# Kernel tuning notes

Measured on AMD Instinct MI355X. Metric: run time of the kernel, lower is better.

Reference implementation:

```python
import jax, jax.numpy as jnp
import numpy as np

N_HEADS = 16


def setup_inputs() -> dict:
    key = jax.random.key(0)
    k1, k2, k3, k4 = jax.random.split(key, 4)
    b, s, d = 2, 2048, 1024
    x = jax.random.normal(k1, (b, s, d), dtype=jnp.float32)
    attn_B = jax.random.normal(k2, (b, N_HEADS, s, s), dtype=jnp.float32) * 0.02
    W_attn = jax.random.normal(k3, (d, 3 * d), dtype=jnp.float32) * (1.0 / np.sqrt(d))
    b_attn = jax.random.normal(k4, (3 * d,), dtype=jnp.float32) * 0.01
    return {"x": x, "attn_B": attn_B, "W_attn": W_attn, "b_attn": b_attn}


def reference(x, attn_B, W_attn, b_attn):
    b, s, d = x.shape
    h = N_HEADS
    hd = d // h
    qkv = x @ W_attn + b_attn                       # [b, s, 3d]
    Q, K, V = jnp.split(qkv, 3, axis=-1)
    # [b, s, d] -> [b, h, s, hd]
    Q = Q.reshape(b, s, h, hd).transpose(0, 2, 1, 3)
    K = K.reshape(b, s, h, hd).transpose(0, 2, 1, 3)
    V = V.reshape(b, s, h, hd).transpose(0, 2, 1, 3)
    scale = 1.0 / jnp.sqrt(jnp.asarray(hd, dtype=Q.dtype))
    scores = jnp.einsum("bhqk,bhsk->bhqs", Q, K) * scale   # [b, h, s, s]
    attn = jax.nn.softmax(scores, axis=-1) + attn_B          # post-softmax additive bias
    y = jnp.einsum("bhqs,bhsd->bhqd", attn, V)               # [b, h, s, hd]
    y = y.transpose(0, 2, 1, 3).reshape(b, s, d)
    return y
```

## Files before the change

kernel.cpp:

```cpp
#include <hip/hip_runtime.h>
#include <hip/hip_bf16.h>


typedef __attribute__((ext_vector_type(4))) float  f32x4;
typedef __attribute__((ext_vector_type(8))) short  bf16x8;
typedef __attribute__((ext_vector_type(4))) short  s16x4;
typedef __attribute__((ext_vector_type(4))) unsigned u32x4;

__device__ __forceinline__ short f2bf(float f) {
    __hip_bfloat16 h = __float2bfloat16(f);
    return __builtin_bit_cast(short, h);
}

__device__ __forceinline__ unsigned cvt_pk_bf16(float lo, float hi) {
    unsigned w;
    asm("v_cvt_pk_bf16_f32 %0, %1, %2" : "=v"(w) : "v"(lo), "v"(hi));
    return w;
}

__device__ __forceinline__ void gll16(const short* g, short* l) {
    __builtin_amdgcn_global_load_lds(
        (const __attribute__((address_space(1))) void*)g,
        (__attribute__((address_space(3))) void*)l, 16, 0, 0);
}

__global__ void conv_x_kernel(const float* __restrict__ x, short* __restrict__ xb) {
    int idx = blockIdx.x * 256 + threadIdx.x;
    f32x4 v = *reinterpret_cast<const f32x4*>(x + (size_t)idx * 4);
    s16x4 o;
    o[0] = f2bf(v[0]); o[1] = f2bf(v[1]); o[2] = f2bf(v[2]); o[3] = f2bf(v[3]);
    *reinterpret_cast<s16x4*>(xb + (size_t)idx * 4) = o;
}

__global__ void wtrans_kernel(const float* __restrict__ W, short* __restrict__ Wt) {
    __shared__ float tile[64][65];
    int kb = blockIdx.x, nb = blockIdx.y;
    int t = threadIdx.x;
    int c4 = (t & 15) * 4;
    int r0 = t >> 4;
#pragma unroll
    for (int rr = 0; rr < 4; ++rr) {
        int kl = r0 + rr * 16;
        f32x4 v = *reinterpret_cast<const f32x4*>(W + (size_t)(kb * 64 + kl) * 3072 + nb * 64 + c4);
        tile[kl][c4 + 0] = v[0]; tile[kl][c4 + 1] = v[1];
        tile[kl][c4 + 2] = v[2]; tile[kl][c4 + 3] = v[3];
    }
    __syncthreads();
#pragma unroll
    for (int rr = 0; rr < 4; ++rr) {
        int nl = r0 + rr * 16;
        s16x4 o;
#pragma unroll
        for (int i = 0; i < 4; ++i) o[i] = f2bf(tile[c4 + i][nl]);
        *reinterpret_cast<s16x4*>(Wt + (size_t)(nb * 64 + nl) * 1024 + kb * 64 + c4) = o;
    }
}

__global__ __launch_bounds__(256) void qkv_gemm_kernel(
    const short* __restrict__ xb, const short* __restrict__ Wt,
    const float* __restrict__ bias,
    short* __restrict__ Qo, short* __restrict__ Ko, short* __restrict__ Vo)
{
    __shared__ short As[128 * 64];
    __shared__ short Bs[128 * 64];
    int tid = threadIdx.x;
    int wave = tid >> 6, lane = tid & 63, g = lane >> 4, lr = lane & 15;
    int wr = wave >> 1, wc = wave & 1;
    int bm = blockIdx.x, bn = blockIdx.y;

    f32x4 acc[4][4];
#pragma unroll
    for (int a = 0; a < 4; ++a)
#pragma unroll
        for (int b = 0; b < 4; ++b) acc[a][b] = (f32x4){0.f, 0.f, 0.f, 0.f};

    for (int k0 = 0; k0 < 1024; k0 += 64) {
#pragma unroll
        for (int j = 0; j < 4; ++j) {
            int c = j * 256 + tid;
            int row = c >> 3, cc = c & 7;
            int scc = (cc ^ (row & 7)) * 8;
            gll16(xb + (size_t)(bm * 128 + row) * 1024 + k0 + scc,
                  &As[(j * 256 + wave * 64) * 8]);
            gll16(Wt + (size_t)(bn * 128 + row) * 1024 + k0 + scc,
                  &Bs[(j * 256 + wave * 64) * 8]);
        }
        __syncthreads();

        bf16x8 af[2][4], bfr[2][4];
#pragma unroll
        for (int mt = 0; mt < 4; ++mt) {
            int row = wr * 64 + mt * 16 + lr;
            af[0][mt] = *reinterpret_cast<const bf16x8*>(&As[row * 64 + (((g    ) ^ (lr & 7)) * 8)]);
            af[1][mt] = *reinterpret_cast<const bf16x8*>(&As[row * 64 + (((g + 4) ^ (lr & 7)) * 8)]);
        }
#pragma unroll
        for (int nt = 0; nt < 4; ++nt) {
            int row = wc * 64 + nt * 16 + lr;
            bfr[0][nt] = *reinterpret_cast<const bf16x8*>(&Bs[row * 64 + (((g    ) ^ (lr & 7)) * 8)]);
            bfr[1][nt] = *reinterpret_cast<const bf16x8*>(&Bs[row * 64 + (((g + 4) ^ (lr & 7)) * 8)]);
        }
#pragma unroll
        for (int mt = 0; mt < 4; ++mt)
#pragma unroll
            for (int nt = 0; nt < 4; ++nt) {
                acc[mt][nt] = __builtin_amdgcn_mfma_f32_16x16x32_bf16(af[0][mt], bfr[0][nt], acc[mt][nt], 0, 0, 0);
                acc[mt][nt] = __builtin_amdgcn_mfma_f32_16x16x32_bf16(af[1][mt], bfr[1][nt], acc[mt][nt], 0, 0, 0);
            }
        __syncthreads();
    }

#pragma unroll
    for (int nt = 0; nt < 4; ++nt) {
        int n = bn * 128 + wc * 64 + nt * 16 + lr;
        float bv = bias[n];
        int which = n >> 10;
        int h = (n >> 6) & 15;
        int dd = n & 63;
        short* base = (which == 0) ? Qo : (which == 1) ? Ko : Vo;
#pragma unroll
        for (int mt = 0; mt < 4; ++mt) {
#pragma unroll
            for (int r = 0; r < 4; ++r) {
                int m = bm * 128 + wr * 64 + mt * 16 + g * 4 + r;
                int bb = m >> 11, s = m & 2047;
                float v = acc[mt][nt][r] + bv;
                base[(((size_t)bb * 16 + h) * 2048 + s) * 64 + dd] = f2bf(v);
            }
        }
    }
}

__global__ __launch_bounds__(256) void vtrans_kernel(const short* __restrict__ V, short* __restrict__ Vt) {
    __shared__ short t[64][72];
    int st = blockIdx.x, bh = blockIdx.y;
    int tid = threadIdx.x;
#pragma unroll
    for (int j = 0; j < 2; ++j) {
        int c = j * 256 + tid;
        int row = c >> 3, cc = c & 7;
        bf16x8 v = *reinterpret_cast<const bf16x8*>(V + (size_t)((bh * 2048) + st * 64 + row) * 64 + cc * 8);
        *reinterpret_cast<bf16x8*>(&t[row][cc * 8]) = v;
    }
    __syncthreads();
#pragma unroll
    for (int j = 0; j < 2; ++j) {
        int c = j * 256 + tid;
        int d = c >> 3, cs = c & 7;
        bf16x8 o;
#pragma unroll
        for (int i = 0; i < 8; ++i) o[i] = t[cs * 8 + i][d];
        *reinterpret_cast<bf16x8*>(Vt + (size_t)(bh * 64 + d) * 2048 + st * 64 + cs * 8) = o;
    }
}

__global__ __launch_bounds__(512, 4) void attn_kernel(
    const short* __restrict__ Qw, const short* __restrict__ Kw, const short* __restrict__ Vtw,
    const float* __restrict__ attnB, float* __restrict__ out)
{
    __shared__ short Ks [2][64 * 64];
    __shared__ short Vts[2][64 * 64];
    __shared__ short Ps [8][16 * 64];

    int id = blockIdx.x;
    int bh3 = id & 7;
    int qt  = (id >> 3) & 15;
    int bh  = ((id >> 7) << 3) | bh3;
    int b = bh >> 4, h = bh & 15;
    int tid = threadIdx.x;
    int wave = tid >> 6, lane = tid & 63, g = lane >> 4, lr = lane & 15;

    const short* Qb = Qw  + (size_t)bh * 2048 * 64;
    const short* Kb = Kw  + (size_t)bh * 2048 * 64;
    const short* Vb = Vtw + (size_t)bh * 64 * 2048;
    const float* Bp = attnB + (size_t)bh * 2048 * 2048;

    int qbase = qt * 128 + wave * 16;

    bf16x8 qf0, qf1;
    {
        const short* qp = Qb + (size_t)(qbase + lr) * 64 + g * 8;
        qf0 = *reinterpret_cast<const bf16x8*>(qp);
        qf1 = *reinterpret_cast<const bf16x8*>(qp + 32);
    }
    const float* brow = Bp + (size_t)(qbase + lr) * 2048 + g * 8;

    f32x4 Os[4], Ob[4];
#pragma unroll
    for (int dt = 0; dt < 4; ++dt) { Os[dt] = (f32x4){0.f,0.f,0.f,0.f}; Ob[dt] = (f32x4){0.f,0.f,0.f,0.f}; }
    float lsum = 0.f;

#define STAGE_KV(buf, ktt) do {                                                   \
    int row = tid >> 3, cc = tid & 7;                                             \
    int scc = (cc ^ (row & 7)) * 8;                                               \
    gll16(Kb + (size_t)((ktt) * 64 + row) * 64 + scc,                             \
          &Ks[buf][wave * 512]);                                                  \
    gll16(Vb + (size_t)row * 2048 + (ktt) * 64 + scc,                             \
          &Vts[buf][wave * 512]);                                                 \
} while (0)

    f32x4 bfn0, bfn1, bfn2, bfn3;
    STAGE_KV(0, 0);
    __builtin_amdgcn_sched_barrier(0);
    bfn0 = __builtin_nontemporal_load(reinterpret_cast<const f32x4*>(brow));
    bfn1 = __builtin_nontemporal_load(reinterpret_cast<const f32x4*>(brow + 4));
    bfn2 = __builtin_nontemporal_load(reinterpret_cast<const f32x4*>(brow + 32));
    bfn3 = __builtin_nontemporal_load(reinterpret_cast<const f32x4*>(brow + 36));
    asm volatile("s_waitcnt vmcnt(4)" ::: "memory");
    __builtin_amdgcn_s_barrier();
    __builtin_amdgcn_sched_barrier(0);

    for (int kt = 0; kt < 32; ++kt) {
        int cur = kt & 1;

        unsigned bb0 = cvt_pk_bf16(bfn0[0], bfn0[1]);
        unsigned bb1 = cvt_pk_bf16(bfn0[2], bfn0[3]);
        unsigned bb2 = cvt_pk_bf16(bfn1[0], bfn1[1]);
        unsigned bb3 = cvt_pk_bf16(bfn1[2], bfn1[3]);
        unsigned bb4 = cvt_pk_bf16(bfn2[0], bfn2[1]);
        unsigned bb5 = cvt_pk_bf16(bfn2[2], bfn2[3]);
        unsigned bb6 = cvt_pk_bf16(bfn3[0], bfn3[1]);
        unsigned bb7 = cvt_pk_bf16(bfn3[2], bfn3[3]);

        if (kt < 31) {
            STAGE_KV(cur ^ 1, kt + 1);
            __builtin_amdgcn_sched_barrier(0);
            const float* bp = brow + (kt + 1) * 64;
            bfn0 = __builtin_nontemporal_load(reinterpret_cast<const f32x4*>(bp));
            bfn1 = __builtin_nontemporal_load(reinterpret_cast<const f32x4*>(bp + 4));
            bfn2 = __builtin_nontemporal_load(reinterpret_cast<const f32x4*>(bp + 32));
            bfn3 = __builtin_nontemporal_load(reinterpret_cast<const f32x4*>(bp + 36));
        }

        f32x4 S[4];
        __builtin_amdgcn_s_setprio(1);
#pragma unroll
        for (int nt = 0; nt < 4; ++nt) {
            int row = nt * 16 + lr;
            bf16x8 kf0 = *reinterpret_cast<const bf16x8*>(&Ks[cur][row * 64 + (((g    ) ^ (lr & 7)) * 8)]);
            bf16x8 kf1 = *reinterpret_cast<const bf16x8*>(&Ks[cur][row * 64 + (((g + 4) ^ (lr & 7)) * 8)]);
            f32x4 s = (f32x4){0.f,0.f,0.f,0.f};
            s = __builtin_amdgcn_mfma_f32_16x16x32_bf16(kf0, qf0, s, 0, 0, 0);
            s = __builtin_amdgcn_mfma_f32_16x16x32_bf16(kf1, qf1, s, 0, 0, 0);
            S[nt] = s;
        }
        __builtin_amdgcn_s_setprio(0);

#pragma unroll
        for (int nt = 0; nt < 4; ++nt)
#pragma unroll
            for (int r = 0; r < 4; ++r) {
                float p = exp2f(S[nt][r] * 0.1803368801111f);
                S[nt][r] = p;
                lsum += p;
            }

        short* psw = &Ps[wave][lr * 64];
#pragma unroll
        for (int nt = 0; nt < 4; ++nt)
#pragma unroll
            for (int rp = 0; rp < 2; ++rp) {
                unsigned w = cvt_pk_bf16(S[nt][2 * rp], S[nt][2 * rp + 1]);
                int kp = 8 * nt + 2 * g + rp;
                int bi = kp >> 2, off = kp & 3;
                *reinterpret_cast<unsigned*>(psw + ((bi ^ (lr & 7)) << 3) + off * 2) = w;
            }

        bf16x8 pf0 = *reinterpret_cast<const bf16x8*>(&Ps[wave][lr * 64 + (((g    ) ^ (lr & 7)) * 8)]);
        bf16x8 pf1 = *reinterpret_cast<const bf16x8*>(&Ps[wave][lr * 64 + (((g + 4) ^ (lr & 7)) * 8)]);
        bf16x8 bbf0, bbf1;
        {
            u32x4 t0 = (u32x4){bb0, bb1, bb2, bb3};
            u32x4 t1 = (u32x4){bb4, bb5, bb6, bb7};
            bbf0 = __builtin_bit_cast(bf16x8, t0);
            bbf1 = __builtin_bit_cast(bf16x8, t1);
        }

        __builtin_amdgcn_s_setprio(1);
#pragma unroll
        for (int dt = 0; dt < 4; ++dt) {
            int row = dt * 16 + lr;
            bf16x8 v0 = *reinterpret_cast<const bf16x8*>(&Vts[cur][row * 64 + (((g    ) ^ (lr & 7)) * 8)]);
            bf16x8 v1 = *reinterpret_cast<const bf16x8*>(&Vts[cur][row * 64 + (((g + 4) ^ (lr & 7)) * 8)]);
            Os[dt] = __builtin_amdgcn_mfma_f32_16x16x32_bf16(pf0,  v0, Os[dt], 0, 0, 0);
            Os[dt] = __builtin_amdgcn_mfma_f32_16x16x32_bf16(pf1,  v1, Os[dt], 0, 0, 0);
            Ob[dt] = __builtin_amdgcn_mfma_f32_16x16x32_bf16(bbf0, v0, Ob[dt], 0, 0, 0);
            Ob[dt] = __builtin_amdgcn_mfma_f32_16x16x32_bf16(bbf1, v1, Ob[dt], 0, 0, 0);
        }
        __builtin_amdgcn_s_setprio(0);

        if (kt < 31) {
            asm volatile("s_waitcnt vmcnt(4)" ::: "memory");
            __builtin_amdgcn_s_barrier();
            __builtin_amdgcn_sched_barrier(0);
        }
    }
#undef STAGE_KV

    float l = lsum;
    l += __shfl_xor(l, 16);
    l += __shfl_xor(l, 32);
    float inv = 1.0f / l;
#pragma unroll
    for (int r = 0; r < 4; ++r) {
        float invr = __shfl(inv, g * 4 + r);
        int q = qbase + g * 4 + r;
#pragma unroll
        for (int dt = 0; dt < 4; ++dt) {
            int dcol = dt * 16 + lr;
            float v = Os[dt][r] * invr + Ob[dt][r];
            __builtin_nontemporal_store(v, &out[((size_t)(b * 2048 + q) * 16 + h) * 64 + dcol]);
        }
    }
}

extern "C" void kernel_launch(void* const* d_in, const int* in_sizes, int n_in,
                              void* d_out, int out_size, void* d_ws, size_t ws_size,
                              hipStream_t stream) {
    const float* x     = (const float*)d_in[0];
    const float* attnB = (const float*)d_in[1];
    const float* W     = (const float*)d_in[2];
    const float* bias  = (const float*)d_in[3];
    float* out = (float*)d_out;

    short* ws = (short*)d_ws;
    short* xb = ws;
    short* Wt = xb + 4194304;
    short* Q  = Wt + 3145728;
    short* K  = Q  + 4194304;
    short* V  = K  + 4194304;
    short* Vt = V  + 4194304;

    conv_x_kernel<<<4096, 256, 0, stream>>>(x, xb);
    wtrans_kernel<<<dim3(16, 48), 256, 0, stream>>>(W, Wt);
    qkv_gemm_kernel<<<dim3(32, 24), 256, 0, stream>>>(xb, Wt, bias, Q, K, V);
    vtrans_kernel<<<dim3(32, 32), 256, 0, stream>>>(V, Vt);
    attn_kernel<<<512, 512, 0, stream>>>(Q, K, Vt, attnB, out);
}
```

Measured before the change: 205.5 us.

## Split bias-times-V product into separate blocks of a heterogeneous fused launch

The attention kernel previously streamed the large fp32 attn_B tensor inside the softmax loop and did the B·V MFMAs alongside P·V. Now one launch of 768 blocks runs two kinds of work. The first 512 blocks do only the softmax attention, and the other 256 blocks do the bias·V product as a plain GEMM into a workspace buffer. A new add kernel then sums the two outputs. This aims to decouple the bandwidth-bound bias stream from the compute-bound attention so they overlap across CUs, at the cost of an extra output round trip and one more launch.

```diff
diff --git a/kernel.cpp b/kernel.cpp
--- a/kernel.cpp
+++ b/kernel.cpp
@@ -16,6 +16,12 @@
     unsigned w;
     asm("v_cvt_pk_bf16_f32 %0, %1, %2" : "=v"(w) : "v"(lo), "v"(hi));
     return w;
+}
+
+__device__ __forceinline__ bf16x8 pack8(f32x4 a, f32x4 b) {
+    u32x4 t = (u32x4){cvt_pk_bf16(a[0], a[1]), cvt_pk_bf16(a[2], a[3]),
+                      cvt_pk_bf16(b[0], b[1]), cvt_pk_bf16(b[2], b[3])};
+    return __builtin_bit_cast(bf16x8, t);
 }
 
 __device__ __forceinline__ void gll16(const short* g, short* l) {
@@ -154,164 +160,234 @@
     }
 }
 
-__global__ __launch_bounds__(512, 4) void attn_kernel(
+__global__ __launch_bounds__(512, 4) void fused_kernel(
     const short* __restrict__ Qw, const short* __restrict__ Kw, const short* __restrict__ Vtw,
-    const float* __restrict__ attnB, float* __restrict__ out)
+    const float* __restrict__ attnB, float* __restrict__ out, float* __restrict__ Obuf)
 {
     __shared__ short Ks [2][64 * 64];
     __shared__ short Vts[2][64 * 64];
     __shared__ short Ps [8][16 * 64];
 
     int id = blockIdx.x;
-    int bh3 = id & 7;
-    int qt  = (id >> 3) & 15;
-    int bh  = ((id >> 7) << 3) | bh3;
-    int b = bh >> 4, h = bh & 15;
     int tid = threadIdx.x;
     int wave = tid >> 6, lane = tid & 63, g = lane >> 4, lr = lane & 15;
 
-    const short* Qb = Qw  + (size_t)bh * 2048 * 64;
-    const short* Kb = Kw  + (size_t)bh * 2048 * 64;
-    const short* Vb = Vtw + (size_t)bh * 64 * 2048;
-    const float* Bp = attnB + (size_t)bh * 2048 * 2048;
-
-    int qbase = qt * 128 + wave * 16;
-
-    bf16x8 qf0, qf1;
-    {
-        const short* qp = Qb + (size_t)(qbase + lr) * 64 + g * 8;
-        qf0 = *reinterpret_cast<const bf16x8*>(qp);
-        qf1 = *reinterpret_cast<const bf16x8*>(qp + 32);
-    }
-    const float* brow = Bp + (size_t)(qbase + lr) * 2048 + g * 8;
-
-    f32x4 Os[4], Ob[4];
-#pragma unroll
-    for (int dt = 0; dt < 4; ++dt) { Os[dt] = (f32x4){0.f,0.f,0.f,0.f}; Ob[dt] = (f32x4){0.f,0.f,0.f,0.f}; }
-    float lsum = 0.f;
+    if (id < 512) {
+        int bh3 = id & 7;
+        int qt  = (id >> 3) & 15;
+        int bh  = ((id >> 7) << 3) | bh3;
+        int b = bh >> 4, h = bh & 15;
+
+        const short* Qb = Qw  + (size_t)bh * 2048 * 64;
+        const short* Kb = Kw  + (size_t)bh * 2048 * 64;
+        const short* Vb = Vtw + (size_t)bh * 64 * 2048;
+
+        int qbase = qt * 128 + wave * 16;
+
+        bf16x8 qf0, qf1;
+        {
+            const short* qp = Qb + (size_t)(qbase + lr) * 64 + g * 8;
+            qf0 = *reinterpret_cast<const bf16x8*>(qp);
+            qf1 = *reinterpret_cast<const bf16x8*>(qp + 32);
+        }
+
+        f32x4 Os[4];
+#pragma unroll
+        for (int dt = 0; dt < 4; ++dt) Os[dt] = (f32x4){0.f,0.f,0.f,0.f};
+        float lsum = 0.f;
 
 #define STAGE_KV(buf, ktt) do {                                                   \
-    int row = tid >> 3, cc = tid & 7;                                             \
-    int scc = (cc ^ (row & 7)) * 8;                                               \
-    gll16(Kb + (size_t)((ktt) * 64 + row) * 64 + scc,                             \
-          &Ks[buf][wave * 512]);                                                  \
-    gll16(Vb + (size_t)row * 2048 + (ktt) * 64 + scc,                             \
-          &Vts[buf][wave * 512]);                                                 \
-} while (0)
-
-    f32x4 bfn0, bfn1, bfn2, bfn3;
-    STAGE_KV(0, 0);
-    __builtin_amdgcn_sched_barrier(0);
-    bfn0 = __builtin_nontemporal_load(reinterpret_cast<const f32x4*>(brow));
-    bfn1 = __builtin_nontemporal_load(reinterpret_cast<const f32x4*>(brow + 4));
-    bfn2 = __builtin_nontemporal_load(reinterpret_cast<const f32x4*>(brow + 32));
-    bfn3 = __builtin_nontemporal_load(reinterpret_cast<const f32x4*>(brow + 36));
-    asm volatile("s_waitcnt vmcnt(4)" ::: "memory");
-    __builtin_amdgcn_s_barrier();
-    __builtin_amdgcn_sched_barrier(0);
-
-    for (int kt = 0; kt < 32; ++kt) {
-        int cur = kt & 1;
-
-        unsigned bb0 = cvt_pk_bf16(bfn0[0], bfn0[1]);
-        unsigned bb1 = cvt_pk_bf16(bfn0[2], bfn0[3]);
-        unsigned bb2 = cvt_pk_bf16(bfn1[0], bfn1[1]);
-        unsigned bb3 = cvt_pk_bf16(bfn1[2], bfn1[3]);
-        unsigned bb4 = cvt_pk_bf16(bfn2[0], bfn2[1]);
-        unsigned bb5 = cvt_pk_bf16(bfn2[2], bfn2[3]);
-        unsigned bb6 = cvt_pk_bf16(bfn3[0], bfn3[1]);
-        unsigned bb7 = cvt_pk_bf16(bfn3[2], bfn3[3]);
-
-        if (kt < 31) {
-            STAGE_KV(cur ^ 1, kt + 1);
+        int row = tid >> 3, cc = tid & 7;                                         \
+        int scc = (cc ^ (row & 7)) * 8;                                           \
+        gll16(Kb + (size_t)((ktt) * 64 + row) * 64 + scc,                         \
+              &Ks[buf][wave * 512]);                                              \
+        gll16(Vb + (size_t)row * 2048 + (ktt) * 64 + scc,                         \
+              &Vts[buf][wave * 512]);                                             \
+    } while (0)
+
+        STAGE_KV(0, 0);
+        asm volatile("s_waitcnt vmcnt(0)" ::: "memory");
+        __builtin_amdgcn_s_barrier();
+        __builtin_amdgcn_sched_barrier(0);
+
+        for (int kt = 0; kt < 32; ++kt) {
+            int cur = kt & 1;
+            if (kt < 31) STAGE_KV(cur ^ 1, kt + 1);
             __builtin_amdgcn_sched_barrier(0);
-            const float* bp = brow + (kt + 1) * 64;
-            bfn0 = __builtin_nontemporal_load(reinterpret_cast<const f32x4*>(bp));
-            bfn1 = __builtin_nontemporal_load(reinterpret_cast<const f32x4*>(bp + 4));
-            bfn2 = __builtin_nontemporal_load(reinterpret_cast<const f32x4*>(bp + 32));
-            bfn3 = __builtin_nontemporal_load(reinterpret_cast<const f32x4*>(bp + 36));
-        }
-
-        f32x4 S[4];
-        __builtin_amdgcn_s_setprio(1);
-#pragma unroll
-        for (int nt = 0; nt < 4; ++nt) {
-            int row = nt * 16 + lr;
-            bf16x8 kf0 = *reinterpret_cast<const bf16x8*>(&Ks[cur][row * 64 + (((g    ) ^ (lr & 7)) * 8)]);
-            bf16x8 kf1 = *reinterpret_cast<const bf16x8*>(&Ks[cur][row * 64 + (((g + 4) ^ (lr & 7)) * 8)]);
-            f32x4 s = (f32x4){0.f,0.f,0.f,0.f};
-            s = __builtin_amdgcn_mfma_f32_16x16x32_bf16(kf0, qf0, s, 0, 0, 0);
-            s = __builtin_amdgcn_mfma_f32_16x16x32_bf16(kf1, qf1, s, 0, 0, 0);
-            S[nt] = s;
-        }
-        __builtin_amdgcn_s_setprio(0);
-
-#pragma unroll
-        for (int nt = 0; nt < 4; ++nt)
-#pragma unroll
-            for (int r = 0; r < 4; ++r) {
-                float p = exp2f(S[nt][r] * 0.1803368801111f);
-                S[nt][r] = p;
-                lsum += p;
-            }
-
-        short* psw = &Ps[wave][lr * 64];
-#pragma unroll
-        for (int nt = 0; nt < 4; ++nt)
-#pragma unroll
-            for (int rp = 0; rp < 2; ++rp) {
-                unsigned w = cvt_pk_bf16(S[nt][2 * rp], S[nt][2 * rp + 1]);
-                int kp = 8 * nt + 2 * g + rp;
-                int bi = kp >> 2, off = kp & 3;
-                *reinterpret_cast<unsigned*>(psw + ((bi ^ (lr & 7)) << 3) + off * 2) = w;
-            }
-
-        bf16x8 pf0 = *reinterpret_cast<const bf16x8*>(&Ps[wave][lr * 64 + (((g    ) ^ (lr & 7)) * 8)]);
-        bf16x8 pf1 = *reinterpret_cast<const bf16x8*>(&Ps[wave][lr * 64 + (((g + 4) ^ (lr & 7)) * 8)]);
-        bf16x8 bbf0, bbf1;
-        {
-            u32x4 t0 = (u32x4){bb0, bb1, bb2, bb3};
-            u32x4 t1 = (u32x4){bb4, bb5, bb6, bb7};
-            bbf0 = __builtin_bit_cast(bf16x8, t0);
-            bbf1 = __builtin_bit_cast(bf16x8, t1);
-        }
-
-        __builtin_amdgcn_s_setprio(1);
-#pragma unroll
-        for (int dt = 0; dt < 4; ++dt) {
-            int row = dt * 16 + lr;
-            bf16x8 v0 = *reinterpret_cast<const bf16x8*>(&Vts[cur][row * 64 + (((g    ) ^ (lr & 7)) * 8)]);
-            bf16x8 v1 = *reinterpret_cast<const bf16x8*>(&Vts[cur][row * 64 + (((g + 4) ^ (lr & 7)) * 8)]);
-            Os[dt] = __builtin_amdgcn_mfma_f32_16x16x32_bf16(pf0,  v0, Os[dt], 0, 0, 0);
-            Os[dt] = __builtin_amdgcn_mfma_f32_16x16x32_bf16(pf1,  v1, Os[dt], 0, 0, 0);
-            Ob[dt] = __builtin_amdgcn_mfma_f32_16x16x32_bf16(bbf0, v0, Ob[dt], 0, 0, 0);
-            Ob[dt] = __builtin_amdgcn_mfma_f32_16x16x32_bf16(bbf1, v1, Ob[dt], 0, 0, 0);
-        }
-        __builtin_amdgcn_s_setprio(0);
-
-        if (kt < 31) {
-            asm volatile("s_waitcnt vmcnt(4)" ::: "memory");
-            __builtin_amdgcn_s_barrier();
-            __builtin_amdgcn_sched_barrier(0);
-        }
-    }
+
+            f32x4 S[4];
+            __builtin_amdgcn_s_setprio(1);
+#pragma unroll
+            for (int nt = 0; nt < 4; ++nt) {
+                int row = nt * 16 + lr;
+                bf16x8 kf0 = *reinterpret_cast<const bf16x8*>(&Ks[cur][row * 64 + (((g    ) ^ (lr & 7)) * 8)]);
+                bf16x8 kf1 = *reinterpret_cast<const bf16x8*>(&Ks[cur][row * 64 + (((g + 4) ^ (lr & 7)) * 8)]);
+                f32x4 s = (f32x4){0.f,0.f,0.f,0.f};
+                s = __builtin_amdgcn_mfma_f32_16x16x32_bf16(kf0, qf0, s, 0, 0, 0);
+                s = __builtin_amdgcn_mfma_f32_16x16x32_bf16(kf1, qf1, s, 0, 0, 0);
+                S[nt] = s;
+            }
+            __builtin_amdgcn_s_setprio(0);
+
+#pragma unroll
+            for (int nt = 0; nt < 4; ++nt)
+#pragma unroll
+                for (int r = 0; r < 4; ++r) {
+                    float p = exp2f(S[nt][r] * 0.1803368801111f);
+                    S[nt][r] = p;
+                    lsum += p;
+                }
+
+            short* psw = &Ps[wave][lr * 64];
+#pragma unroll
+            for (int nt = 0; nt < 4; ++nt)
+#pragma unroll
+                for (int rp = 0; rp < 2; ++rp) {
+                    unsigned w = cvt_pk_bf16(S[nt][2 * rp], S[nt][2 * rp + 1]);
+                    int kp = 8 * nt + 2 * g + rp;
+                    int bi = kp >> 2, off = kp & 3;
+                    *reinterpret_cast<unsigned*>(psw + ((bi ^ (lr & 7)) << 3) + off * 2) = w;
+                }
+
+            bf16x8 pf0 = *reinterpret_cast<const bf16x8*>(&Ps[wave][lr * 64 + (((g    ) ^ (lr & 7)) * 8)]);
+            bf16x8 pf1 = *reinterpret_cast<const bf16x8*>(&Ps[wave][lr * 64 + (((g + 4) ^ (lr & 7)) * 8)]);
+
+            __builtin_amdgcn_s_setprio(1);
+#pragma unroll
+            for (int dt = 0; dt < 4; ++dt) {
+                int row = dt * 16 + lr;
+                bf16x8 v0 = *reinterpret_cast<const bf16x8*>(&Vts[cur][row * 64 + (((g    ) ^ (lr & 7)) * 8)]);
+                bf16x8 v1 = *reinterpret_cast<const bf16x8*>(&Vts[cur][row * 64 + (((g + 4) ^ (lr & 7)) * 8)]);
+                Os[dt] = __builtin_amdgcn_mfma_f32_16x16x32_bf16(pf0, v0, Os[dt], 0, 0, 0);
+                Os[dt] = __builtin_amdgcn_mfma_f32_16x16x32_bf16(pf1, v1, Os[dt], 0, 0, 0);
+            }
+            __builtin_amdgcn_s_setprio(0);
+
+            if (kt < 31) {
+                asm volatile("s_waitcnt vmcnt(0)" ::: "memory");
+                __builtin_amdgcn_s_barrier();
+                __builtin_amdgcn_sched_barrier(0);
+            }
+        }
 #undef STAGE_KV
 
-    float l = lsum;
-    l += __shfl_xor(l, 16);
-    l += __shfl_xor(l, 32);
-    float inv = 1.0f / l;
-#pragma unroll
-    for (int r = 0; r < 4; ++r) {
-        float invr = __shfl(inv, g * 4 + r);
-        int q = qbase + g * 4 + r;
-#pragma unroll
-        for (int dt = 0; dt < 4; ++dt) {
-            int dcol = dt * 16 + lr;
-            float v = Os[dt][r] * invr + Ob[dt][r];
-            __builtin_nontemporal_store(v, &out[((size_t)(b * 2048 + q) * 16 + h) * 64 + dcol]);
-        }
-    }
+        float l = lsum;
+        l += __shfl_xor(l, 16);
+        l += __shfl_xor(l, 32);
+        float inv = 1.0f / l;
+#pragma unroll
+        for (int r = 0; r < 4; ++r) {
+            float invr = __shfl(inv, g * 4 + r);
+            int q = qbase + g * 4 + r;
+#pragma unroll
+            for (int dt = 0; dt < 4; ++dt) {
+                int dcol = dt * 16 + lr;
+                out[((size_t)(b * 2048 + q) * 16 + h) * 64 + dcol] = Os[dt][r] * invr;
+            }
+        }
+    } else {
+        int j = id - 512;
+        int bh = ((j >> 6) << 3) | (j & 7);
+        int qt2 = (j >> 3) & 7;
+        int b = bh >> 4, h = bh & 15;
+        int qb = qt2 * 256;
+
+        const float* Bp = attnB + (size_t)bh * 2048 * 2048;
+        const short* Vb = Vtw + (size_t)bh * 64 * 2048;
+        const float* br0 = Bp + (size_t)(qb + wave * 32 + lr) * 2048 + g * 8;
+        const float* br1 = br0 + (size_t)16 * 2048;
+
+        f32x4 acc[2][4];
+#pragma unroll
+        for (int mt = 0; mt < 2; ++mt)
+#pragma unroll
+            for (int nt = 0; nt < 4; ++nt) acc[mt][nt] = (f32x4){0.f,0.f,0.f,0.f};
+
+#define STAGE_V(buf, ktt) do {                                                    \
+        int row = tid >> 3, cc = tid & 7;                                         \
+        int scc = (cc ^ (row & 7)) * 8;                                           \
+        gll16(Vb + (size_t)row * 2048 + (ktt) * 64 + scc,                         \
+              &Ks[buf][wave * 512]);                                              \
+    } while (0)
+
+        f32x4 b00, b01, b02, b03, b10, b11, b12, b13;
+        STAGE_V(0, 0);
+        __builtin_amdgcn_sched_barrier(0);
+        b00 = __builtin_nontemporal_load(reinterpret_cast<const f32x4*>(br0));
+        b01 = __builtin_nontemporal_load(reinterpret_cast<const f32x4*>(br0 + 4));
+        b02 = __builtin_nontemporal_load(reinterpret_cast<const f32x4*>(br0 + 32));
+        b03 = __builtin_nontemporal_load(reinterpret_cast<const f32x4*>(br0 + 36));
+        b10 = __builtin_nontemporal_load(reinterpret_cast<const f32x4*>(br1));
+        b11 = __builtin_nontemporal_load(reinterpret_cast<const f32x4*>(br1 + 4));
+        b12 = __builtin_nontemporal_load(reinterpret_cast<const f32x4*>(br1 + 32));
+        b13 = __builtin_nontemporal_load(reinterpret_cast<const f32x4*>(br1 + 36));
+        asm volatile("s_waitcnt vmcnt(8)" ::: "memory");
+        __builtin_amdgcn_s_barrier();
+        __builtin_amdgcn_sched_barrier(0);
+
+        for (int kt = 0; kt < 32; ++kt) {
+            int cur = kt & 1;
+
+            bf16x8 a00 = pack8(b00, b01);
+            bf16x8 a01 = pack8(b02, b03);
+            bf16x8 a10 = pack8(b10, b11);
+            bf16x8 a11 = pack8(b12, b13);
+
+            if (kt < 31) {
+                STAGE_V(cur ^ 1, kt + 1);
+                __builtin_amdgcn_sched_barrier(0);
+                const float* p0 = br0 + (kt + 1) * 64;
+                const float* p1 = br1 + (kt + 1) * 64;
+                b00 = __builtin_nontemporal_load(reinterpret_cast<const f32x4*>(p0));
+                b01 = __builtin_nontemporal_load(reinterpret_cast<const f32x4*>(p0 + 4));
+                b02 = __builtin_nontemporal_load(reinterpret_cast<const f32x4*>(p0 + 32));
+                b03 = __builtin_nontemporal_load(reinterpret_cast<const f32x4*>(p0 + 36));
+                b10 = __builtin_nontemporal_load(reinterpret_cast<const f32x4*>(p1));
+                b11 = __builtin_nontemporal_load(reinterpret_cast<const f32x4*>(p1 + 4));
+                b12 = __builtin_nontemporal_load(reinterpret_cast<const f32x4*>(p1 + 32));
+                b13 = __builtin_nontemporal_load(reinterpret_cast<const f32x4*>(p1 + 36));
+            }
+
+            __builtin_amdgcn_s_setprio(1);
+#pragma unroll
+            for (int nt = 0; nt < 4; ++nt) {
+                int row = nt * 16 + lr;
+                bf16x8 v0 = *reinterpret_cast<const bf16x8*>(&Ks[cur][row * 64 + (((g    ) ^ (lr & 7)) * 8)]);
+                bf16x8 v1 = *reinterpret_cast<const bf16x8*>(&Ks[cur][row * 64 + (((g + 4) ^ (lr & 7)) * 8)]);
+                acc[0][nt] = __builtin_amdgcn_mfma_f32_16x16x32_bf16(a00, v0, acc[0][nt], 0, 0, 0);
+                acc[0][nt] = __builtin_amdgcn_mfma_f32_16x16x32_bf16(a01, v1, acc[0][nt], 0, 0, 0);
+                acc[1][nt] = __builtin_amdgcn_mfma_f32_16x16x32_bf16(a10, v0, acc[1][nt], 0, 0, 0);
+                acc[1][nt] = __builtin_amdgcn_mfma_f32_16x16x32_bf16(a11, v1, acc[1][nt], 0, 0, 0);
+            }
+            __builtin_amdgcn_s_setprio(0);
+
+            if (kt < 31) {
+                asm volatile("s_waitcnt vmcnt(8)" ::: "memory");
+                __builtin_amdgcn_s_barrier();
+                __builtin_amdgcn_sched_barrier(0);
+            }
+        }
+#undef STAGE_V
+
+#pragma unroll
+        for (int mt = 0; mt < 2; ++mt)
+#pragma unroll
+            for (int nt = 0; nt < 4; ++nt)
+#pragma unroll
+                for (int r = 0; r < 4; ++r) {
+                    int q = qb + wave * 32 + mt * 16 + g * 4 + r;
+                    int d = nt * 16 + lr;
+                    Obuf[((size_t)(b * 2048 + q) * 16 + h) * 64 + d] = acc[mt][nt][r];
+                }
+    }
+}
+
+__global__ void add_kernel(float* __restrict__ out, const float* __restrict__ Obuf) {
+    int idx = blockIdx.x * 256 + threadIdx.x;
+    f32x4 a = *reinterpret_cast<const f32x4*>(out + (size_t)idx * 4);
+    f32x4 c = *reinterpret_cast<const f32x4*>(Obuf + (size_t)idx * 4);
+    a[0] += c[0]; a[1] += c[1]; a[2] += c[2]; a[3] += c[3];
+    *reinterpret_cast<f32x4*>(out + (size_t)idx * 4) = a;
 }
 
 extern "C" void kernel_launch(void* const* d_in, const int* in_sizes, int n_in,
@@ -330,10 +406,12 @@
     short* K  = Q  + 4194304;
     short* V  = K  + 4194304;
     short* Vt = V  + 4194304;
+    float* Obuf = (float*)(Vt + 4194304);
 
     conv_x_kernel<<<4096, 256, 0, stream>>>(x, xb);
     wtrans_kernel<<<dim3(16, 48), 256, 0, stream>>>(W, Wt);
     qkv_gemm_kernel<<<dim3(32, 24), 256, 0, stream>>>(xb, Wt, bias, Q, K, V);
     vtrans_kernel<<<dim3(32, 32), 256, 0, stream>>>(V, Vt);
-    attn_kernel<<<512, 512, 0, stream>>>(Q, K, Vt, attnB, out);
-}
+    fused_kernel<<<768, 512, 0, stream>>>(Q, K, Vt, attnB, out, Obuf);
+    add_kernel<<<4096, 256, 0, stream>>>(out, Obuf);
+}
```

New measurement: 264.5 us. 28.7% more time.

## Fuse V transpose into QKV GEMM epilogue and deepen bias prefetch in attention

Applied to the files above, without the earlier changes.

The QKV GEMM epilogue now writes V directly in transposed [bh, d, s] layout using 4-element vector stores, so the separate vtrans kernel launch and its extra round trip through memory go away. The attention loop is unrolled by two with static buffer indices, and the attn_B bias tiles are prefetched two iterations ahead using regular loads instead of nontemporal ones. This is meant to hide the bias memory latency better. The cost is more live registers under launch_bounds(512,4), and the vmcnt accounting becomes more delicate.

```diff
diff --git a/kernel.cpp b/kernel.cpp
--- a/kernel.cpp
+++ b/kernel.cpp
@@ -16,6 +16,12 @@
     unsigned w;
     asm("v_cvt_pk_bf16_f32 %0, %1, %2" : "=v"(w) : "v"(lo), "v"(hi));
     return w;
+}
+
+__device__ __forceinline__ bf16x8 pack8(f32x4 a, f32x4 b) {
+    u32x4 t = (u32x4){cvt_pk_bf16(a[0], a[1]), cvt_pk_bf16(a[2], a[3]),
+                      cvt_pk_bf16(b[0], b[1]), cvt_pk_bf16(b[2], b[3])};
+    return __builtin_bit_cast(bf16x8, t);
 }
 
 __device__ __forceinline__ void gll16(const short* g, short* l) {
@@ -59,7 +65,7 @@
 __global__ __launch_bounds__(256) void qkv_gemm_kernel(
     const short* __restrict__ xb, const short* __restrict__ Wt,
     const float* __restrict__ bias,
-    short* __restrict__ Qo, short* __restrict__ Ko, short* __restrict__ Vo)
+    short* __restrict__ Qo, short* __restrict__ Ko, short* __restrict__ Vto)
 {
     __shared__ short As[128 * 64];
     __shared__ short Bs[128 * 64];
@@ -117,40 +123,24 @@
         int which = n >> 10;
         int h = (n >> 6) & 15;
         int dd = n & 63;
-        short* base = (which == 0) ? Qo : (which == 1) ? Ko : Vo;
 #pragma unroll
         for (int mt = 0; mt < 4; ++mt) {
-#pragma unroll
-            for (int r = 0; r < 4; ++r) {
-                int m = bm * 128 + wr * 64 + mt * 16 + g * 4 + r;
-                int bb = m >> 11, s = m & 2047;
-                float v = acc[mt][nt][r] + bv;
-                base[(((size_t)bb * 16 + h) * 2048 + s) * 64 + dd] = f2bf(v);
-            }
-        }
-    }
-}
-
-__global__ __launch_bounds__(256) void vtrans_kernel(const short* __restrict__ V, short* __restrict__ Vt) {
-    __shared__ short t[64][72];
-    int st = blockIdx.x, bh = blockIdx.y;
-    int tid = threadIdx.x;
-#pragma unroll
-    for (int j = 0; j < 2; ++j) {
-        int c = j * 256 + tid;
-        int row = c >> 3, cc = c & 7;
-        bf16x8 v = *reinterpret_cast<const bf16x8*>(V + (size_t)((bh * 2048) + st * 64 + row) * 64 + cc * 8);
-        *reinterpret_cast<bf16x8*>(&t[row][cc * 8]) = v;
-    }
-    __syncthreads();
-#pragma unroll
-    for (int j = 0; j < 2; ++j) {
-        int c = j * 256 + tid;
-        int d = c >> 3, cs = c & 7;
-        bf16x8 o;
-#pragma unroll
-        for (int i = 0; i < 8; ++i) o[i] = t[cs * 8 + i][d];
-        *reinterpret_cast<bf16x8*>(Vt + (size_t)(bh * 64 + d) * 2048 + st * 64 + cs * 8) = o;
+            int m0 = bm * 128 + wr * 64 + mt * 16 + g * 4;
+            int bb = m0 >> 11, s0 = m0 & 2047;
+            if (which == 2) {
+                s16x4 o;
+#pragma unroll
+                for (int r = 0; r < 4; ++r) o[r] = f2bf(acc[mt][nt][r] + bv);
+                *reinterpret_cast<s16x4*>(
+                    Vto + ((size_t)(bb * 16 + h) * 64 + dd) * 2048 + s0) = o;
+            } else {
+                short* base = (which == 0) ? Qo : Ko;
+#pragma unroll
+                for (int r = 0; r < 4; ++r)
+                    base[(((size_t)bb * 16 + h) * 2048 + s0 + r) * 64 + dd] =
+                        f2bf(acc[mt][nt][r] + bv);
+            }
+        }
     }
 }
 
@@ -199,103 +189,110 @@
           &Vts[buf][wave * 512]);                                                 \
 } while (0)
 
-    f32x4 bfn0, bfn1, bfn2, bfn3;
+#define LOADB(d0, d1, d2, d3, ktt) do {                                           \
+    const float* bp_ = brow + (size_t)(ktt) * 64;                                 \
+    d0 = *reinterpret_cast<const f32x4*>(bp_);                                    \
+    d1 = *reinterpret_cast<const f32x4*>(bp_ + 4);                                \
+    d2 = *reinterpret_cast<const f32x4*>(bp_ + 32);                               \
+    d3 = *reinterpret_cast<const f32x4*>(bp_ + 36);                               \
+} while (0)
+
+#define COMPUTE(cur, xb0, xb1) do {                                               \
+    f32x4 S[4];                                                                   \
+    __builtin_amdgcn_s_setprio(1);                                                \
+    _Pragma("unroll")                                                             \
+    for (int nt = 0; nt < 4; ++nt) {                                              \
+        int row = nt * 16 + lr;                                                   \
+        bf16x8 kf0 = *reinterpret_cast<const bf16x8*>(&Ks[cur][row * 64 + (((g    ) ^ (lr & 7)) * 8)]); \
+        bf16x8 kf1 = *reinterpret_cast<const bf16x8*>(&Ks[cur][row * 64 + (((g + 4) ^ (lr & 7)) * 8)]); \
+        f32x4 s = (f32x4){0.f,0.f,0.f,0.f};                                       \
+        s = __builtin_amdgcn_mfma_f32_16x16x32_bf16(kf0, qf0, s, 0, 0, 0);        \
+        s = __builtin_amdgcn_mfma_f32_16x16x32_bf16(kf1, qf1, s, 0, 0, 0);        \
+        S[nt] = s;                                                                \
+    }                                                                             \
+    __builtin_amdgcn_s_setprio(0);                                                \
+    _Pragma("unroll")                                                             \
+    for (int nt = 0; nt < 4; ++nt)                                                \
+        _Pragma("unroll")                                                         \
+        for (int r = 0; r < 4; ++r) {                                             \
+            float p = exp2f(S[nt][r] * 0.1803368801111f);                         \
+            S[nt][r] = p;                                                         \
+            lsum += p;                                                            \
+        }                                                                         \
+    short* psw = &Ps[wave][lr * 64];                                              \
+    _Pragma("unroll")                                                             \
+    for (int nt = 0; nt < 4; ++nt)                                                \
+        _Pragma("unroll")                                                         \
+        for (int rp = 0; rp < 2; ++rp) {                                          \
+            unsigned w = cvt_pk_bf16(S[nt][2 * rp], S[nt][2 * rp + 1]);           \
+            int kp = 8 * nt + 2 * g + rp;                                         \
+            int bi = kp >> 2, off = kp & 3;                                       \
+            *reinterpret_cast<unsigned*>(psw + ((bi ^ (lr & 7)) << 3) + off * 2) = w; \
+        }                                                                         \
+    bf16x8 pf0 = *reinterpret_cast<const bf16x8*>(&Ps[wave][lr * 64 + (((g    ) ^ (lr & 7)) * 8)]); \
+    bf16x8 pf1 = *reinterpret_cast<const bf16x8*>(&Ps[wave][lr * 64 + (((g + 4) ^ (lr & 7)) * 8)]); \
+    __builtin_amdgcn_s_setprio(1);                                                \
+    _Pragma("unroll")                                                             \
+    for (int dt = 0; dt < 4; ++dt) {                                              \
+        int row = dt * 16 + lr;                                                   \
+        bf16x8 v0 = *reinterpret_cast<const bf16x8*>(&Vts[cur][row * 64 + (((g    ) ^ (lr & 7)) * 8)]); \
+        bf16x8 v1 = *reinterpret_cast<const bf16x8*>(&Vts[cur][row * 64 + (((g + 4) ^ (lr & 7)) * 8)]); \
+        Os[dt] = __builtin_amdgcn_mfma_f32_16x16x32_bf16(pf0, v0, Os[dt], 0, 0, 0); \
+        Os[dt] = __builtin_amdgcn_mfma_f32_16x16x32_bf16(pf1, v1, Os[dt], 0, 0, 0); \
+        Ob[dt] = __builtin_amdgcn_mfma_f32_16x16x32_bf16(xb0, v0, Ob[dt], 0, 0, 0); \
+        Ob[dt] = __builtin_amdgcn_mfma_f32_16x16x32_bf16(xb1, v1, Ob[dt], 0, 0, 0); \
+    }                                                                             \
+    __builtin_amdgcn_s_setprio(0);                                                \
+} while (0)
+
+    f32x4 a0, a1, a2, a3, p0, p1, p2, p3;
+
     STAGE_KV(0, 0);
     __builtin_amdgcn_sched_barrier(0);
-    bfn0 = __builtin_nontemporal_load(reinterpret_cast<const f32x4*>(brow));
-    bfn1 = __builtin_nontemporal_load(reinterpret_cast<const f32x4*>(brow + 4));
-    bfn2 = __builtin_nontemporal_load(reinterpret_cast<const f32x4*>(brow + 32));
-    bfn3 = __builtin_nontemporal_load(reinterpret_cast<const f32x4*>(brow + 36));
-    asm volatile("s_waitcnt vmcnt(4)" ::: "memory");
+    LOADB(a0, a1, a2, a3, 0);
+    LOADB(p0, p1, p2, p3, 1);
+    __builtin_amdgcn_sched_barrier(0);
+    asm volatile("s_waitcnt vmcnt(8)" ::: "memory");
     __builtin_amdgcn_s_barrier();
     __builtin_amdgcn_sched_barrier(0);
 
-    for (int kt = 0; kt < 32; ++kt) {
-        int cur = kt & 1;
-
-        unsigned bb0 = cvt_pk_bf16(bfn0[0], bfn0[1]);
-        unsigned bb1 = cvt_pk_bf16(bfn0[2], bfn0[3]);
-        unsigned bb2 = cvt_pk_bf16(bfn1[0], bfn1[1]);
-        unsigned bb3 = cvt_pk_bf16(bfn1[2], bfn1[3]);
-        unsigned bb4 = cvt_pk_bf16(bfn2[0], bfn2[1]);
-        unsigned bb5 = cvt_pk_bf16(bfn2[2], bfn2[3]);
-        unsigned bb6 = cvt_pk_bf16(bfn3[0], bfn3[1]);
-        unsigned bb7 = cvt_pk_bf16(bfn3[2], bfn3[3]);
-
-        if (kt < 31) {
-            STAGE_KV(cur ^ 1, kt + 1);
+    for (int t = 0; t < 16; ++t) {
+        {
+            bf16x8 bbf0 = pack8(a0, a1);
+            bf16x8 bbf1 = pack8(a2, a3);
+            STAGE_KV(1, 2 * t + 1);
             __builtin_amdgcn_sched_barrier(0);
-            const float* bp = brow + (kt + 1) * 64;
-            bfn0 = __builtin_nontemporal_load(reinterpret_cast<const f32x4*>(bp));
-            bfn1 = __builtin_nontemporal_load(reinterpret_cast<const f32x4*>(bp + 4));
-            bfn2 = __builtin_nontemporal_load(reinterpret_cast<const f32x4*>(bp + 32));
-            bfn3 = __builtin_nontemporal_load(reinterpret_cast<const f32x4*>(bp + 36));
-        }
-
-        f32x4 S[4];
-        __builtin_amdgcn_s_setprio(1);
-#pragma unroll
-        for (int nt = 0; nt < 4; ++nt) {
-            int row = nt * 16 + lr;
-            bf16x8 kf0 = *reinterpret_cast<const bf16x8*>(&Ks[cur][row * 64 + (((g    ) ^ (lr & 7)) * 8)]);
-            bf16x8 kf1 = *reinterpret_cast<const bf16x8*>(&Ks[cur][row * 64 + (((g + 4) ^ (lr & 7)) * 8)]);
-            f32x4 s = (f32x4){0.f,0.f,0.f,0.f};
-            s = __builtin_amdgcn_mfma_f32_16x16x32_bf16(kf0, qf0, s, 0, 0, 0);
-            s = __builtin_amdgcn_mfma_f32_16x16x32_bf16(kf1, qf1, s, 0, 0, 0);
-            S[nt] = s;
-        }
-        __builtin_amdgcn_s_setprio(0);
-
-#pragma unroll
-        for (int nt = 0; nt < 4; ++nt)
-#pragma unroll
-            for (int r = 0; r < 4; ++r) {
-                float p = exp2f(S[nt][r] * 0.1803368801111f);
-                S[nt][r] = p;
-                lsum += p;
-            }
-
-        short* psw = &Ps[wave][lr * 64];
-#pragma unroll
-        for (int nt = 0; nt < 4; ++nt)
-#pragma unroll
-            for (int rp = 0; rp < 2; ++rp) {
-                unsigned w = cvt_pk_bf16(S[nt][2 * rp], S[nt][2 * rp + 1]);
-                int kp = 8 * nt + 2 * g + rp;
-                int bi = kp >> 2, off = kp & 3;
-                *reinterpret_cast<unsigned*>(psw + ((bi ^ (lr & 7)) << 3) + off * 2) = w;
-            }
-
-        bf16x8 pf0 = *reinterpret_cast<const bf16x8*>(&Ps[wave][lr * 64 + (((g    ) ^ (lr & 7)) * 8)]);
-        bf16x8 pf1 = *reinterpret_cast<const bf16x8*>(&Ps[wave][lr * 64 + (((g + 4) ^ (lr & 7)) * 8)]);
-        bf16x8 bbf0, bbf1;
-        {
-            u32x4 t0 = (u32x4){bb0, bb1, bb2, bb3};
-            u32x4 t1 = (u32x4){bb4, bb5, bb6, bb7};
-            bbf0 = __builtin_bit_cast(bf16x8, t0);
-            bbf1 = __builtin_bit_cast(bf16x8, t1);
-        }
-
-        __builtin_amdgcn_s_setprio(1);
-#pragma unroll
-        for (int dt = 0; dt < 4; ++dt) {
-            int row = dt * 16 + lr;
-            bf16x8 v0 = *reinterpret_cast<const bf16x8*>(&Vts[cur][row * 64 + (((g    ) ^ (lr & 7)) * 8)]);
-            bf16x8 v1 = *reinterpret_cast<const bf16x8*>(&Vts[cur][row * 64 + (((g + 4) ^ (lr & 7)) * 8)]);
-            Os[dt] = __builtin_amdgcn_mfma_f32_16x16x32_bf16(pf0,  v0, Os[dt], 0, 0, 0);
-            Os[dt] = __builtin_amdgcn_mfma_f32_16x16x32_bf16(pf1,  v1, Os[dt], 0, 0, 0);
-            Ob[dt] = __builtin_amdgcn_mfma_f32_16x16x32_bf16(bbf0, v0, Ob[dt], 0, 0, 0);
-            Ob[dt] = __builtin_amdgcn_mfma_f32_16x16x32_bf16(bbf1, v1, Ob[dt], 0, 0, 0);
-        }
-        __builtin_amdgcn_s_setprio(0);
-
-        if (kt < 31) {
-            asm volatile("s_waitcnt vmcnt(4)" ::: "memory");
+            if (t < 15) LOADB(a0, a1, a2, a3, 2 * t + 2);
+            __builtin_amdgcn_sched_barrier(0);
+            COMPUTE(0, bbf0, bbf1);
+            if (t < 15) {
+                asm volatile("s_waitcnt vmcnt(4)" ::: "memory");
+            } else {
+                asm volatile("s_waitcnt vmcnt(0)" ::: "memory");
+            }
             __builtin_amdgcn_s_barrier();
             __builtin_amdgcn_sched_barrier(0);
         }
+        {
+            bf16x8 bbf0 = pack8(p0, p1);
+            bf16x8 bbf1 = pack8(p2, p3);
+            if (t < 15) {
+                STAGE_KV(0, 2 * t + 2);
+                __builtin_amdgcn_sched_barrier(0);
+                LOADB(p0, p1, p2, p3, 2 * t + 3);
+                __builtin_amdgcn_sched_barrier(0);
+            }
+            COMPUTE(1, bbf0, bbf1);
+            if (t < 15) {
+                asm volatile("s_waitcnt vmcnt(4)" ::: "memory");
+                __builtin_amdgcn_s_barrier();
+                __builtin_amdgcn_sched_barrier(0);
+            }
+        }
     }
 #undef STAGE_KV
+#undef LOADB
+#undef COMPUTE
 
     float l = lsum;
     l += __shfl_xor(l, 16);
@@ -328,12 +325,10 @@
     short* Wt = xb + 4194304;
     short* Q  = Wt + 3145728;
     short* K  = Q  + 4194304;
-    short* V  = K  + 4194304;
-    short* Vt = V  + 4194304;
+    short* Vt = K  + 4194304;
 
     conv_x_kernel<<<4096, 256, 0, stream>>>(x, xb);
     wtrans_kernel<<<dim3(16, 48), 256, 0, stream>>>(W, Wt);
-    qkv_gemm_kernel<<<dim3(32, 24), 256, 0, stream>>>(xb, Wt, bias, Q, K, V);
-    vtrans_kernel<<<dim3(32, 32), 256, 0, stream>>>(V, Vt);
+    qkv_gemm_kernel<<<dim3(32, 24), 256, 0, stream>>>(xb, Wt, bias, Q, K, Vt);
     attn_kernel<<<512, 512, 0, stream>>>(Q, K, Vt, attnB, out);
 }
```

Result: no change. 208.1 us (+1.3%).
